# Performance work log

Hardware: AMD Instinct MI355X
Metric: run time of the kernel (lower is better)

The kernel has to match this reference:

```python
import jax, jax.numpy as jnp
import numpy as np

B, C_IN, C_MID, C_OUT, R, K = 2048, 64, 64, 128, 60, 13
EPS = 1e-5


def _gather(x, nei):
    # x: [B, C, 60] -> gather neighbors -> [B, C, 60, 13]
    b, c = x.shape[0], x.shape[1]
    return x[:, :, nei].reshape(b, c, R, K)


def _block(x, nei, g, bta, m, v, W, c):
    # BN (eval mode) -> ReLU -> Conv2d(kernel (1,13)) fused block.
    h = _gather(x, nei)                              # [B,C,60,13]
    inv = g * jax.lax.rsqrt(v + EPS)                 # [C]
    h = jax.nn.relu(h * inv[None, :, None, None] + (bta - m * inv)[None, :, None, None])
    # Conv2d with kernel (1,13), stride 1 == contraction over (c, k)
    return jnp.einsum('bcrk,ock->bor', h, W) + c[None, :, None]  # [B,O,60]


def setup_inputs() -> dict:
    key = jax.random.key(0)
    ks = jax.random.split(key, 24)
    n = lambda k, s: jax.random.normal(k, s, dtype=jnp.float32)
    u = lambda k, s: jax.random.uniform(k, s, dtype=jnp.float32, minval=0.5, maxval=1.5)
    return {
        "x": n(ks[0], (B, C_IN, R)),
        "nei": jax.random.randint(ks[1], (R * K,), 0, R, dtype=jnp.int32),
        # comb_layer_in: BN(in) + Conv(in->mid)
        "g1": n(ks[2], (C_IN,)), "b1": n(ks[3], (C_IN,)), "m1": n(ks[4], (C_IN,)), "v1": u(ks[5], (C_IN,)),
        "W1": n(ks[6], (C_MID, C_IN, K)) * 0.1, "c1": n(ks[7], (C_MID,)) * 0.1,
        # comb_layer_out: BN(mid) + Conv(mid->out)
        "g2": n(ks[8], (C_MID,)), "b2": n(ks[9], (C_MID,)), "m2": n(ks[10], (C_MID,)), "v2": u(ks[11], (C_MID,)),
        "W2": n(ks[12], (C_OUT, C_MID, K)) * 0.1, "c2": n(ks[13], (C_OUT,)) * 0.1,
        # short_cut_layer: BN(in) + Conv(in->out)
        "g3": n(ks[14], (C_IN,)), "b3": n(ks[15], (C_IN,)), "m3": n(ks[16], (C_IN,)), "v3": u(ks[17], (C_IN,)),
        "W3": n(ks[18], (C_OUT, C_IN, K)) * 0.1, "c3": n(ks[19], (C_OUT,)) * 0.1,
    }


def reference(x, nei, g1, b1, m1, v1, W1, c1, g2, b2, m2, v2, W2, c2,
              g3, b3, m3, v3, W3, c3):
    f = _block(x, nei, g1, b1, m1, v1, W1, c1)      # [B, C_MID, 60]
    f = _block(f, nei, g2, b2, m2, v2, W2, c2)      # [B, C_OUT, 60]
    sc = _block(x, nei, g3, b3, m3, v3, W3, c3)     # [B, C_OUT, 60]
    return f + sc
```

## Files before the change

kernel.cpp:

```cpp
#include <hip/hip_runtime.h>
#include <hip/hip_bf16.h>


typedef __attribute__((ext_vector_type(8))) short bf16x8;
typedef __attribute__((ext_vector_type(4))) float f32x4;
typedef __attribute__((ext_vector_type(4))) unsigned short us4;

#define EPSV 1e-5f
#define ZSTRIDE 72
#define ZCOLBYTES 144
#define ZELEMS (64 * ZSTRIDE)

__device__ __forceinline__ unsigned short f2bf(float f) {
  unsigned int u = __builtin_bit_cast(unsigned int, f);
  u += 0x7FFFu + ((u >> 16) & 1u);
  return (unsigned short)(u >> 16);
}

__global__ void prep_w(const float* __restrict__ W1, const float* __restrict__ W2,
                       const float* __restrict__ W3, unsigned short* __restrict__ W1t,
                       unsigned short* __restrict__ W23t) {
  int gid = blockIdx.x * 256 + threadIdx.x;
  if (gid < 64 * 832) {
    int o = gid / 832;
    int kk = gid - o * 832;
    int ks = kk >> 6, c = kk & 63;
    W1t[gid] = f2bf(W1[(o * 64 + c) * 13 + ks]);
  } else {
    int idx = gid - 64 * 832;
    int o = idx / 1664;
    int kk = idx - o * 1664;
    int kq = kk >> 6, c = kk & 63;
    float v = (kq < 13) ? W2[(o * 64 + c) * 13 + kq] : W3[(o * 64 + c) * 13 + (kq - 13)];
    W23t[idx] = f2bf(v);
  }
}

#define MFMA __builtin_amdgcn_mfma_f32_16x16x32_bf16

__global__ __launch_bounds__(256, 2) void fused_k(
    const float* __restrict__ x, const int* __restrict__ nei,
    const float* __restrict__ g1, const float* __restrict__ be1,
    const float* __restrict__ mu1, const float* __restrict__ va1,
    const float* __restrict__ c1,
    const float* __restrict__ g2, const float* __restrict__ be2,
    const float* __restrict__ mu2, const float* __restrict__ va2,
    const float* __restrict__ c2,
    const float* __restrict__ g3, const float* __restrict__ be3,
    const float* __restrict__ mu3, const float* __restrict__ va3,
    const float* __restrict__ c3,
    const unsigned short* __restrict__ W1t,
    const unsigned short* __restrict__ W23t,
    float* __restrict__ out)
{
  __shared__ unsigned short z1[ZELEMS];
  __shared__ unsigned short zz[2 * ZELEMS];
  __shared__ int lneio[780];
  __shared__ float pp[6 * 64];
  __shared__ float pcc[128];

  const int tid  = threadIdx.x;
  const int wave = tid >> 6;
  const int lane = tid & 63;
  const int quad = lane >> 4;
  const int nl   = lane & 15;

  if (tid < 64) {
    float a1v = g1[tid] * rsqrtf(va1[tid] + EPSV);
    pp[tid]       = a1v;
    pp[64 + tid]  = be1[tid] - mu1[tid] * a1v;
    float a2v = g2[tid] * rsqrtf(va2[tid] + EPSV);
    pp[128 + tid] = a2v;
    pp[192 + tid] = be2[tid] - mu2[tid] * a2v + a2v * c1[tid];
    float a3v = g3[tid] * rsqrtf(va3[tid] + EPSV);
    pp[256 + tid] = a3v;
    pp[320 + tid] = be3[tid] - mu3[tid] * a3v;
  } else if (tid >= 128) {
    pcc[tid - 128] = c2[tid - 128] + c3[tid - 128];
  }
  for (int i = tid; i < 780; i += 256) lneio[i] = nei[i] * ZCOLBYTES;
  __syncthreads();

  const float* xb = x + blockIdx.x * (64 * 60);
  unsigned short* z3p = zz + ZELEMS;
  for (int i = tid; i < 64 * 60; i += 256) {
    int c = i / 60;
    int r = i - c * 60;
    float xv = xb[i];
    z1[r * ZSTRIDE + c]  = f2bf(fmaxf(fmaf(xv, pp[c],       pp[64 + c]),  0.f));
    z3p[r * ZSTRIDE + c] = f2bf(fmaxf(fmaf(xv, pp[256 + c], pp[320 + c]), 0.f));
  }
  __syncthreads();

  int rcl13[4];
  #pragma unroll
  for (int nt = 0; nt < 4; nt++) {
    int r = nt * 16 + nl;
    rcl13[nt] = (r < 60 ? r : 59) * 13;
  }

  f32x4 acc1[4] = {};
  {
    const unsigned short* w1p = W1t + (wave * 16 + nl) * 832 + quad * 8;
    bf16x8 aC0 = *(const bf16x8*)(w1p);
    bf16x8 aC1 = *(const bf16x8*)(w1p + 32);
    const char* zb = (const char*)z1 + quad * 16;
    #pragma unroll 1
    for (int ks = 0; ks < 13; ks++) {
      int pf = (ks < 12 ? ks + 1 : 12) * 64;
      bf16x8 aN0 = *(const bf16x8*)(w1p + pf);
      bf16x8 aN1 = *(const bf16x8*)(w1p + pf + 32);
      int no0 = lneio[rcl13[0] + ks];
      int no1 = lneio[rcl13[1] + ks];
      int no2 = lneio[rcl13[2] + ks];
      int no3 = lneio[rcl13[3] + ks];
      bf16x8 bb;
      bb = *(const bf16x8*)(zb + no0);      acc1[0] = MFMA(aC0, bb, acc1[0], 0, 0, 0);
      bb = *(const bf16x8*)(zb + no1);      acc1[1] = MFMA(aC0, bb, acc1[1], 0, 0, 0);
      bb = *(const bf16x8*)(zb + no2);      acc1[2] = MFMA(aC0, bb, acc1[2], 0, 0, 0);
      bb = *(const bf16x8*)(zb + no3);      acc1[3] = MFMA(aC0, bb, acc1[3], 0, 0, 0);
      bb = *(const bf16x8*)(zb + no0 + 64); acc1[0] = MFMA(aC1, bb, acc1[0], 0, 0, 0);
      bb = *(const bf16x8*)(zb + no1 + 64); acc1[1] = MFMA(aC1, bb, acc1[1], 0, 0, 0);
      bb = *(const bf16x8*)(zb + no2 + 64); acc1[2] = MFMA(aC1, bb, acc1[2], 0, 0, 0);
      bb = *(const bf16x8*)(zb + no3 + 64); acc1[3] = MFMA(aC1, bb, acc1[3], 0, 0, 0);
      aC0 = aN0; aC1 = aN1;
    }
  }

  {
    int ob = wave * 16 + quad * 4;
    float a20 = pp[128 + ob], a21 = pp[128 + ob + 1], a22 = pp[128 + ob + 2], a23 = pp[128 + ob + 3];
    float b20 = pp[192 + ob], b21 = pp[192 + ob + 1], b22 = pp[192 + ob + 2], b23 = pp[192 + ob + 3];
    #pragma unroll
    for (int nt = 0; nt < 4; nt++) {
      int r = nt * 16 + nl;
      us4 w;
      w.x = f2bf(fmaxf(fmaf(acc1[nt][0], a20, b20), 0.f));
      w.y = f2bf(fmaxf(fmaf(acc1[nt][1], a21, b21), 0.f));
      w.z = f2bf(fmaxf(fmaf(acc1[nt][2], a22, b22), 0.f));
      w.w = f2bf(fmaxf(fmaf(acc1[nt][3], a23, b23), 0.f));
      *(us4*)&zz[r * ZSTRIDE + ob] = w;
    }
  }
  __syncthreads();

  f32x4 acc2[8] = {};
  {
    const unsigned short* wp0 = W23t + (wave * 32 + nl) * 1664 + quad * 8;
    const unsigned short* wp1 = wp0 + 16 * 1664;
    bf16x8 a0C0 = *(const bf16x8*)(wp0);
    bf16x8 a0C1 = *(const bf16x8*)(wp0 + 32);
    bf16x8 a1C0 = *(const bf16x8*)(wp1);
    bf16x8 a1C1 = *(const bf16x8*)(wp1 + 32);
    #pragma unroll 1
    for (int kt = 0; kt < 26; kt++) {
      int pf = (kt < 25 ? kt + 1 : 25) * 64;
      bf16x8 n00 = *(const bf16x8*)(wp0 + pf);
      bf16x8 n01 = *(const bf16x8*)(wp0 + pf + 32);
      bf16x8 n10 = *(const bf16x8*)(wp1 + pf);
      bf16x8 n11 = *(const bf16x8*)(wp1 + pf + 32);
      int ks = (kt < 13) ? kt : (kt - 13);
      const char* zb = (const char*)zz + ((kt < 13) ? 0 : 2 * ZELEMS) + quad * 16;
      int no0 = lneio[rcl13[0] + ks];
      int no1 = lneio[rcl13[1] + ks];
      int no2 = lneio[rcl13[2] + ks];
      int no3 = lneio[rcl13[3] + ks];
      bf16x8 bb;
      bb = *(const bf16x8*)(zb + no0);
      acc2[0] = MFMA(a0C0, bb, acc2[0], 0, 0, 0);
      acc2[4] = MFMA(a1C0, bb, acc2[4], 0, 0, 0);
      bb = *(const bf16x8*)(zb + no1);
      acc2[1] = MFMA(a0C0, bb, acc2[1], 0, 0, 0);
      acc2[5] = MFMA(a1C0, bb, acc2[5], 0, 0, 0);
      bb = *(const bf16x8*)(zb + no2);
      acc2[2] = MFMA(a0C0, bb, acc2[2], 0, 0, 0);
      acc2[6] = MFMA(a1C0, bb, acc2[6], 0, 0, 0);
      bb = *(const bf16x8*)(zb + no3);
      acc2[3] = MFMA(a0C0, bb, acc2[3], 0, 0, 0);
      acc2[7] = MFMA(a1C0, bb, acc2[7], 0, 0, 0);
      bb = *(const bf16x8*)(zb + no0 + 64);
      acc2[0] = MFMA(a0C1, bb, acc2[0], 0, 0, 0);
      acc2[4] = MFMA(a1C1, bb, acc2[4], 0, 0, 0);
      bb = *(const bf16x8*)(zb + no1 + 64);
      acc2[1] = MFMA(a0C1, bb, acc2[1], 0, 0, 0);
      acc2[5] = MFMA(a1C1, bb, acc2[5], 0, 0, 0);
      bb = *(const bf16x8*)(zb + no2 + 64);
      acc2[2] = MFMA(a0C1, bb, acc2[2], 0, 0, 0);
      acc2[6] = MFMA(a1C1, bb, acc2[6], 0, 0, 0);
      bb = *(const bf16x8*)(zb + no3 + 64);
      acc2[3] = MFMA(a0C1, bb, acc2[3], 0, 0, 0);
      acc2[7] = MFMA(a1C1, bb, acc2[7], 0, 0, 0);
      a0C0 = n00; a0C1 = n01; a1C0 = n10; a1C1 = n11;
    }
  }

  float* outb = out + blockIdx.x * (128 * 60);
  #pragma unroll
  for (int mt = 0; mt < 2; mt++) {
    int ob = wave * 32 + mt * 16 + quad * 4;
    float q0 = pcc[ob], q1 = pcc[ob + 1], q2 = pcc[ob + 2], q3 = pcc[ob + 3];
    #pragma unroll
    for (int nt = 0; nt < 4; nt++) {
      int r = nt * 16 + nl;
      if (r < 60) {
        f32x4 a = acc2[mt * 4 + nt];
        outb[(ob + 0) * 60 + r] = a[0] + q0;
        outb[(ob + 1) * 60 + r] = a[1] + q1;
        outb[(ob + 2) * 60 + r] = a[2] + q2;
        outb[(ob + 3) * 60 + r] = a[3] + q3;
      }
    }
  }
}

extern "C" void kernel_launch(void* const* d_in, const int* in_sizes, int n_in,
                              void* d_out, int out_size, void* d_ws, size_t ws_size,
                              hipStream_t stream) {
  const float* x   = (const float*)d_in[0];
  const int*   nei = (const int*)d_in[1];
  const float* g1  = (const float*)d_in[2];
  const float* be1 = (const float*)d_in[3];
  const float* mu1 = (const float*)d_in[4];
  const float* va1 = (const float*)d_in[5];
  const float* W1  = (const float*)d_in[6];
  const float* c1  = (const float*)d_in[7];
  const float* g2  = (const float*)d_in[8];
  const float* be2 = (const float*)d_in[9];
  const float* mu2 = (const float*)d_in[10];
  const float* va2 = (const float*)d_in[11];
  const float* W2  = (const float*)d_in[12];
  const float* c2  = (const float*)d_in[13];
  const float* g3  = (const float*)d_in[14];
  const float* be3 = (const float*)d_in[15];
  const float* mu3 = (const float*)d_in[16];
  const float* va3 = (const float*)d_in[17];
  const float* W3  = (const float*)d_in[18];
  const float* c3  = (const float*)d_in[19];

  unsigned short* W1t  = (unsigned short*)d_ws;
  unsigned short* W23t = W1t + 64 * 832;

  prep_w<<<1040, 256, 0, stream>>>(W1, W2, W3, W1t, W23t);
  fused_k<<<2048, 256, 0, stream>>>(x, nei, g1, be1, mu1, va1, c1,
                                    g2, be2, mu2, va2, c2,
                                    g3, be3, mu3, va3, c3,
                                    W1t, W23t, (float*)d_out);
}
```

Measured before the change: 254.8 us.

## Retile MFMA wave work to 2D output tiles and prefetch neighbor offsets

Each wave now owns a 2D tile: in stage 1, 32 output channels by 32 rows, and in stage 2, 64 output channels by 32 rows, instead of a strip of all rows. This halves the gathered B-fragment LDS reads per MFMA, because each B load now feeds 2 or 4 MFMAs, at the cost of loading more weight fragments per wave. Neighbor offsets are prefetched one iteration ahead, and launch bounds rise to 3 blocks per CU, which may squeeze registers. prep_w is rewritten so each thread converts 13 contiguous weights, using far fewer blocks.

```diff
diff --git a/kernel.cpp b/kernel.cpp
--- a/kernel.cpp
+++ b/kernel.cpp
@@ -20,25 +20,27 @@
 __global__ void prep_w(const float* __restrict__ W1, const float* __restrict__ W2,
                        const float* __restrict__ W3, unsigned short* __restrict__ W1t,
                        unsigned short* __restrict__ W23t) {
-  int gid = blockIdx.x * 256 + threadIdx.x;
-  if (gid < 64 * 832) {
-    int o = gid / 832;
-    int kk = gid - o * 832;
-    int ks = kk >> 6, c = kk & 63;
-    W1t[gid] = f2bf(W1[(o * 64 + c) * 13 + ks]);
-  } else {
-    int idx = gid - 64 * 832;
-    int o = idx / 1664;
-    int kk = idx - o * 1664;
-    int kq = kk >> 6, c = kk & 63;
-    float v = (kq < 13) ? W2[(o * 64 + c) * 13 + kq] : W3[(o * 64 + c) * 13 + (kq - 13)];
-    W23t[idx] = f2bf(v);
+  int t = blockIdx.x * 256 + threadIdx.x;
+  if (t < 4096) {
+    int o = t >> 6, c = t & 63;
+    const float* src = W1 + (o * 64 + c) * 13;
+    unsigned short* dst = W1t + o * 832 + c;
+    #pragma unroll
+    for (int ks = 0; ks < 13; ks++) dst[ks * 64] = f2bf(src[ks]);
+  } else if (t < 20480) {
+    int idx = t - 4096;
+    int half = idx >> 13;
+    int o = (idx >> 6) & 127, c = idx & 63;
+    const float* src = (half ? W3 : W2) + (o * 64 + c) * 13;
+    unsigned short* dst = W23t + o * 1664 + half * 13 * 64 + c;
+    #pragma unroll
+    for (int ks = 0; ks < 13; ks++) dst[ks * 64] = f2bf(src[ks]);
   }
 }
 
 #define MFMA __builtin_amdgcn_mfma_f32_16x16x32_bf16
 
-__global__ __launch_bounds__(256, 2) void fused_k(
+__global__ __launch_bounds__(256, 3) void fused_k(
     const float* __restrict__ x, const int* __restrict__ nei,
     const float* __restrict__ g1, const float* __restrict__ be1,
     const float* __restrict__ mu1, const float* __restrict__ va1,
@@ -92,118 +94,135 @@
   }
   __syncthreads();
 
-  int rcl13[4];
-  #pragma unroll
-  for (int nt = 0; nt < 4; nt++) {
-    int r = nt * 16 + nl;
-    rcl13[nt] = (r < 60 ? r : 59) * 13;
-  }
+  const int r0 = (wave & 1) * 32 + nl;
+  const int r1 = r0 + 16;
+  const int r0c13 = (r0 < 60 ? r0 : 59) * 13;
+  const int r1c13 = (r1 < 60 ? r1 : 59) * 13;
 
   f32x4 acc1[4] = {};
   {
-    const unsigned short* w1p = W1t + (wave * 16 + nl) * 832 + quad * 8;
-    bf16x8 aC0 = *(const bf16x8*)(w1p);
-    bf16x8 aC1 = *(const bf16x8*)(w1p + 32);
+    const unsigned short* wpa = W1t + ((wave >> 1) * 32 + nl) * 832 + quad * 8;
+    const unsigned short* wpb = wpa + 16 * 832;
+    bf16x8 a0c0 = *(const bf16x8*)(wpa);
+    bf16x8 a0c1 = *(const bf16x8*)(wpa + 32);
+    bf16x8 a1c0 = *(const bf16x8*)(wpb);
+    bf16x8 a1c1 = *(const bf16x8*)(wpb + 32);
     const char* zb = (const char*)z1 + quad * 16;
+    int no0 = lneio[r0c13];
+    int no1 = lneio[r1c13];
     #pragma unroll 1
     for (int ks = 0; ks < 13; ks++) {
-      int pf = (ks < 12 ? ks + 1 : 12) * 64;
-      bf16x8 aN0 = *(const bf16x8*)(w1p + pf);
-      bf16x8 aN1 = *(const bf16x8*)(w1p + pf + 32);
-      int no0 = lneio[rcl13[0] + ks];
-      int no1 = lneio[rcl13[1] + ks];
-      int no2 = lneio[rcl13[2] + ks];
-      int no3 = lneio[rcl13[3] + ks];
-      bf16x8 bb;
-      bb = *(const bf16x8*)(zb + no0);      acc1[0] = MFMA(aC0, bb, acc1[0], 0, 0, 0);
-      bb = *(const bf16x8*)(zb + no1);      acc1[1] = MFMA(aC0, bb, acc1[1], 0, 0, 0);
-      bb = *(const bf16x8*)(zb + no2);      acc1[2] = MFMA(aC0, bb, acc1[2], 0, 0, 0);
-      bb = *(const bf16x8*)(zb + no3);      acc1[3] = MFMA(aC0, bb, acc1[3], 0, 0, 0);
-      bb = *(const bf16x8*)(zb + no0 + 64); acc1[0] = MFMA(aC1, bb, acc1[0], 0, 0, 0);
-      bb = *(const bf16x8*)(zb + no1 + 64); acc1[1] = MFMA(aC1, bb, acc1[1], 0, 0, 0);
-      bb = *(const bf16x8*)(zb + no2 + 64); acc1[2] = MFMA(aC1, bb, acc1[2], 0, 0, 0);
-      bb = *(const bf16x8*)(zb + no3 + 64); acc1[3] = MFMA(aC1, bb, acc1[3], 0, 0, 0);
-      aC0 = aN0; aC1 = aN1;
+      int ksn = (ks < 12) ? ks + 1 : 12;
+      int non0 = lneio[r0c13 + ksn];
+      int non1 = lneio[r1c13 + ksn];
+      int pf = ksn * 64;
+      bf16x8 n0c0 = *(const bf16x8*)(wpa + pf);
+      bf16x8 n0c1 = *(const bf16x8*)(wpa + pf + 32);
+      bf16x8 n1c0 = *(const bf16x8*)(wpb + pf);
+      bf16x8 n1c1 = *(const bf16x8*)(wpb + pf + 32);
+      bf16x8 b;
+      b = *(const bf16x8*)(zb + no0);
+      acc1[0] = MFMA(a0c0, b, acc1[0], 0, 0, 0);
+      acc1[2] = MFMA(a1c0, b, acc1[2], 0, 0, 0);
+      b = *(const bf16x8*)(zb + no0 + 64);
+      acc1[0] = MFMA(a0c1, b, acc1[0], 0, 0, 0);
+      acc1[2] = MFMA(a1c1, b, acc1[2], 0, 0, 0);
+      b = *(const bf16x8*)(zb + no1);
+      acc1[1] = MFMA(a0c0, b, acc1[1], 0, 0, 0);
+      acc1[3] = MFMA(a1c0, b, acc1[3], 0, 0, 0);
+      b = *(const bf16x8*)(zb + no1 + 64);
+      acc1[1] = MFMA(a0c1, b, acc1[1], 0, 0, 0);
+      acc1[3] = MFMA(a1c1, b, acc1[3], 0, 0, 0);
+      a0c0 = n0c0; a0c1 = n0c1; a1c0 = n1c0; a1c1 = n1c1;
+      no0 = non0; no1 = non1;
     }
   }
 
   {
-    int ob = wave * 16 + quad * 4;
-    float a20 = pp[128 + ob], a21 = pp[128 + ob + 1], a22 = pp[128 + ob + 2], a23 = pp[128 + ob + 3];
-    float b20 = pp[192 + ob], b21 = pp[192 + ob + 1], b22 = pp[192 + ob + 2], b23 = pp[192 + ob + 3];
-    #pragma unroll
-    for (int nt = 0; nt < 4; nt++) {
-      int r = nt * 16 + nl;
-      us4 w;
-      w.x = f2bf(fmaxf(fmaf(acc1[nt][0], a20, b20), 0.f));
-      w.y = f2bf(fmaxf(fmaf(acc1[nt][1], a21, b21), 0.f));
-      w.z = f2bf(fmaxf(fmaf(acc1[nt][2], a22, b22), 0.f));
-      w.w = f2bf(fmaxf(fmaf(acc1[nt][3], a23, b23), 0.f));
-      *(us4*)&zz[r * ZSTRIDE + ob] = w;
+    #pragma unroll
+    for (int mt = 0; mt < 2; mt++) {
+      int ob = (wave >> 1) * 32 + mt * 16 + quad * 4;
+      float a20 = pp[128 + ob],     a21 = pp[128 + ob + 1];
+      float a22 = pp[128 + ob + 2], a23 = pp[128 + ob + 3];
+      float b20 = pp[192 + ob],     b21 = pp[192 + ob + 1];
+      float b22 = pp[192 + ob + 2], b23 = pp[192 + ob + 3];
+      #pragma unroll
+      for (int nt = 0; nt < 2; nt++) {
+        int r = (wave & 1) * 32 + nt * 16 + nl;
+        f32x4 a = acc1[mt * 2 + nt];
+        us4 w;
+        w.x = f2bf(fmaxf(fmaf(a[0], a20, b20), 0.f));
+        w.y = f2bf(fmaxf(fmaf(a[1], a21, b21), 0.f));
+        w.z = f2bf(fmaxf(fmaf(a[2], a22, b22), 0.f));
+        w.w = f2bf(fmaxf(fmaf(a[3], a23, b23), 0.f));
+        *(us4*)&zz[r * ZSTRIDE + ob] = w;
+      }
     }
   }
   __syncthreads();
 
   f32x4 acc2[8] = {};
   {
-    const unsigned short* wp0 = W23t + (wave * 32 + nl) * 1664 + quad * 8;
+    const unsigned short* wp0 = W23t + ((wave >> 1) * 64 + nl) * 1664 + quad * 8;
     const unsigned short* wp1 = wp0 + 16 * 1664;
-    bf16x8 a0C0 = *(const bf16x8*)(wp0);
-    bf16x8 a0C1 = *(const bf16x8*)(wp0 + 32);
-    bf16x8 a1C0 = *(const bf16x8*)(wp1);
-    bf16x8 a1C1 = *(const bf16x8*)(wp1 + 32);
+    const unsigned short* wp2 = wp0 + 32 * 1664;
+    const unsigned short* wp3 = wp0 + 48 * 1664;
+    bf16x8 a0c0 = *(const bf16x8*)(wp0), a0c1 = *(const bf16x8*)(wp0 + 32);
+    bf16x8 a1c0 = *(const bf16x8*)(wp1), a1c1 = *(const bf16x8*)(wp1 + 32);
+    bf16x8 a2c0 = *(const bf16x8*)(wp2), a2c1 = *(const bf16x8*)(wp2 + 32);
+    bf16x8 a3c0 = *(const bf16x8*)(wp3), a3c1 = *(const bf16x8*)(wp3 + 32);
+    const char* zzb = (const char*)zz + quad * 16;
+    int no0 = lneio[r0c13];
+    int no1 = lneio[r1c13];
     #pragma unroll 1
     for (int kt = 0; kt < 26; kt++) {
-      int pf = (kt < 25 ? kt + 1 : 25) * 64;
-      bf16x8 n00 = *(const bf16x8*)(wp0 + pf);
-      bf16x8 n01 = *(const bf16x8*)(wp0 + pf + 32);
-      bf16x8 n10 = *(const bf16x8*)(wp1 + pf);
-      bf16x8 n11 = *(const bf16x8*)(wp1 + pf + 32);
-      int ks = (kt < 13) ? kt : (kt - 13);
-      const char* zb = (const char*)zz + ((kt < 13) ? 0 : 2 * ZELEMS) + quad * 16;
-      int no0 = lneio[rcl13[0] + ks];
-      int no1 = lneio[rcl13[1] + ks];
-      int no2 = lneio[rcl13[2] + ks];
-      int no3 = lneio[rcl13[3] + ks];
-      bf16x8 bb;
-      bb = *(const bf16x8*)(zb + no0);
-      acc2[0] = MFMA(a0C0, bb, acc2[0], 0, 0, 0);
-      acc2[4] = MFMA(a1C0, bb, acc2[4], 0, 0, 0);
-      bb = *(const bf16x8*)(zb + no1);
-      acc2[1] = MFMA(a0C0, bb, acc2[1], 0, 0, 0);
-      acc2[5] = MFMA(a1C0, bb, acc2[5], 0, 0, 0);
-      bb = *(const bf16x8*)(zb + no2);
-      acc2[2] = MFMA(a0C0, bb, acc2[2], 0, 0, 0);
-      acc2[6] = MFMA(a1C0, bb, acc2[6], 0, 0, 0);
-      bb = *(const bf16x8*)(zb + no3);
-      acc2[3] = MFMA(a0C0, bb, acc2[3], 0, 0, 0);
-      acc2[7] = MFMA(a1C0, bb, acc2[7], 0, 0, 0);
-      bb = *(const bf16x8*)(zb + no0 + 64);
-      acc2[0] = MFMA(a0C1, bb, acc2[0], 0, 0, 0);
-      acc2[4] = MFMA(a1C1, bb, acc2[4], 0, 0, 0);
-      bb = *(const bf16x8*)(zb + no1 + 64);
-      acc2[1] = MFMA(a0C1, bb, acc2[1], 0, 0, 0);
-      acc2[5] = MFMA(a1C1, bb, acc2[5], 0, 0, 0);
-      bb = *(const bf16x8*)(zb + no2 + 64);
-      acc2[2] = MFMA(a0C1, bb, acc2[2], 0, 0, 0);
-      acc2[6] = MFMA(a1C1, bb, acc2[6], 0, 0, 0);
-      bb = *(const bf16x8*)(zb + no3 + 64);
-      acc2[3] = MFMA(a0C1, bb, acc2[3], 0, 0, 0);
-      acc2[7] = MFMA(a1C1, bb, acc2[7], 0, 0, 0);
-      a0C0 = n00; a0C1 = n01; a1C0 = n10; a1C1 = n11;
+      int ktn = (kt < 25) ? kt + 1 : 25;
+      int ksn = (ktn < 13) ? ktn : ktn - 13;
+      int non0 = lneio[r0c13 + ksn];
+      int non1 = lneio[r1c13 + ksn];
+      int pf = ktn * 64;
+      bf16x8 n0c0 = *(const bf16x8*)(wp0 + pf), n0c1 = *(const bf16x8*)(wp0 + pf + 32);
+      bf16x8 n1c0 = *(const bf16x8*)(wp1 + pf), n1c1 = *(const bf16x8*)(wp1 + pf + 32);
+      bf16x8 n2c0 = *(const bf16x8*)(wp2 + pf), n2c1 = *(const bf16x8*)(wp2 + pf + 32);
+      bf16x8 n3c0 = *(const bf16x8*)(wp3 + pf), n3c1 = *(const bf16x8*)(wp3 + pf + 32);
+      const char* zb = zzb + ((kt < 13) ? 0 : 2 * ZELEMS);
+      bf16x8 b;
+      b = *(const bf16x8*)(zb + no0);
+      acc2[0] = MFMA(a0c0, b, acc2[0], 0, 0, 0);
+      acc2[2] = MFMA(a1c0, b, acc2[2], 0, 0, 0);
+      acc2[4] = MFMA(a2c0, b, acc2[4], 0, 0, 0);
+      acc2[6] = MFMA(a3c0, b, acc2[6], 0, 0, 0);
+      b = *(const bf16x8*)(zb + no0 + 64);
+      acc2[0] = MFMA(a0c1, b, acc2[0], 0, 0, 0);
+      acc2[2] = MFMA(a1c1, b, acc2[2], 0, 0, 0);
+      acc2[4] = MFMA(a2c1, b, acc2[4], 0, 0, 0);
+      acc2[6] = MFMA(a3c1, b, acc2[6], 0, 0, 0);
+      b = *(const bf16x8*)(zb + no1);
+      acc2[1] = MFMA(a0c0, b, acc2[1], 0, 0, 0);
+      acc2[3] = MFMA(a1c0, b, acc2[3], 0, 0, 0);
+      acc2[5] = MFMA(a2c0, b, acc2[5], 0, 0, 0);
+      acc2[7] = MFMA(a3c0, b, acc2[7], 0, 0, 0);
+      b = *(const bf16x8*)(zb + no1 + 64);
+      acc2[1] = MFMA(a0c1, b, acc2[1], 0, 0, 0);
+      acc2[3] = MFMA(a1c1, b, acc2[3], 0, 0, 0);
+      acc2[5] = MFMA(a2c1, b, acc2[5], 0, 0, 0);
+      acc2[7] = MFMA(a3c1, b, acc2[7], 0, 0, 0);
+      a0c0 = n0c0; a0c1 = n0c1; a1c0 = n1c0; a1c1 = n1c1;
+      a2c0 = n2c0; a2c1 = n2c1; a3c0 = n3c0; a3c1 = n3c1;
+      no0 = non0; no1 = non1;
     }
   }
 
   float* outb = out + blockIdx.x * (128 * 60);
   #pragma unroll
-  for (int mt = 0; mt < 2; mt++) {
-    int ob = wave * 32 + mt * 16 + quad * 4;
+  for (int mt = 0; mt < 4; mt++) {
+    int ob = (wave >> 1) * 64 + mt * 16 + quad * 4;
     float q0 = pcc[ob], q1 = pcc[ob + 1], q2 = pcc[ob + 2], q3 = pcc[ob + 3];
     #pragma unroll
-    for (int nt = 0; nt < 4; nt++) {
-      int r = nt * 16 + nl;
+    for (int nt = 0; nt < 2; nt++) {
+      int r = (wave & 1) * 32 + nt * 16 + nl;
       if (r < 60) {
-        f32x4 a = acc2[mt * 4 + nt];
+        f32x4 a = acc2[mt * 2 + nt];
         outb[(ob + 0) * 60 + r] = a[0] + q0;
         outb[(ob + 1) * 60 + r] = a[1] + q1;
         outb[(ob + 2) * 60 + r] = a[2] + q2;
@@ -240,7 +259,7 @@
   unsigned short* W1t  = (unsigned short*)d_ws;
   unsigned short* W23t = W1t + 64 * 832;
 
-  prep_w<<<1040, 256, 0, stream>>>(W1, W2, W3, W1t, W23t);
+  prep_w<<<80, 256, 0, stream>>>(W1, W2, W3, W1t, W23t);
   fused_k<<<2048, 256, 0, stream>>>(x, nei, g1, be1, mu1, va1, c1,
                                     g2, be2, mu2, va2, c2,
                                     g3, be3, mu3, va3, c3,
```

Result: slower. 357.1 us (+40.2%).
